# Performance work log

Hardware: AMD Instinct MI355X
Metric: run time of the kernel (lower is better)

The kernel has to match this reference:

```python
import jax, jax.numpy as jnp
import numpy as np

N, E, F_IN, H, C, G, NCLS, L = 50000, 600000, 128, 4, 64, 64, 3, 3
HC = H * C  # 256


def gatv2_layer(x, src, dst, Wl, bl, Wr, br, att, bias):
    # PyG GATv2Conv (concat=True, negative_slope=0.2, share_weights=False),
    # eval mode so attention dropout is identity.
    n = x.shape[0]
    xl = (x @ Wl + bl).reshape(n, H, C)  # source transform
    xr = (x @ Wr + br).reshape(n, H, C)  # target transform
    e = jax.nn.leaky_relu(xl[src] + xr[dst], negative_slope=0.2)  # [E',H,C]
    score = jnp.einsum('ehc,hc->eh', e, att)                      # [E',H]
    # softmax over incoming edges of each destination node
    mx = jax.ops.segment_max(score, dst, num_segments=n)
    ex = jnp.exp(score - mx[dst])
    denom = jax.ops.segment_sum(ex, dst, num_segments=n)
    alpha = ex / denom[dst]                                       # [E',H]
    out = jax.ops.segment_sum(alpha[..., None] * xl[src], dst, num_segments=n)
    return out.reshape(n, HC) + bias


def setup_inputs() -> dict:
    key = jax.random.key(0)
    ks = jax.random.split(key, 32)
    d = {}
    d['x'] = jax.random.normal(ks[0], (N, F_IN), dtype=jnp.float32)
    d['edge_index'] = jax.random.randint(ks[1], (2, E), 0, N, dtype=jnp.int64)
    d['batch'] = jnp.sort(jax.random.randint(ks[2], (N,), 0, G, dtype=jnp.int64))
    k = 3
    for li in range(L):
        fin = F_IN if li == 0 else HC
        s = 1.0 / np.sqrt(fin)
        d[f'Wl{li}'] = jax.random.normal(ks[k], (fin, HC), dtype=jnp.float32) * s; k += 1
        d[f'bl{li}'] = jnp.zeros((HC,), dtype=jnp.float32)
        d[f'Wr{li}'] = jax.random.normal(ks[k], (fin, HC), dtype=jnp.float32) * s; k += 1
        d[f'br{li}'] = jnp.zeros((HC,), dtype=jnp.float32)
        d[f'att{li}'] = jax.random.normal(ks[k], (H, C), dtype=jnp.float32) * (1.0 / np.sqrt(C)); k += 1
        d[f'bias{li}'] = jnp.zeros((HC,), dtype=jnp.float32)
    d['Wout'] = jax.random.normal(ks[k], (HC, NCLS), dtype=jnp.float32) * (1.0 / np.sqrt(HC))
    d['bout'] = jnp.zeros((NCLS,), dtype=jnp.float32)
    return d


def reference(x, edge_index, batch,
              Wl0, bl0, Wr0, br0, att0, bias0,
              Wl1, bl1, Wr1, br1, att1, bias1,
              Wl2, bl2, Wr2, br2, att2, bias2,
              Wout, bout):
    # add self loops (add_self_loops=True)
    loops = jnp.arange(N, dtype=edge_index.dtype)
    src = jnp.concatenate([edge_index[0], loops])
    dst = jnp.concatenate([edge_index[1], loops])

    h = gatv2_layer(x, src, dst, Wl0, bl0, Wr0, br0, att0, bias0)
    for (Wl, bl, Wr, br, att, bias) in [(Wl1, bl1, Wr1, br1, att1, bias1),
                                        (Wl2, bl2, Wr2, br2, att2, bias2)]:
        h = jax.nn.relu(h)
        h = gatv2_layer(h, src, dst, Wl, bl, Wr, br, att, bias)

    # pooling=0: mean + max over graphs
    counts = jax.ops.segment_sum(jnp.ones((N,), dtype=h.dtype), batch, num_segments=G)
    mean_p = jax.ops.segment_sum(h, batch, num_segments=G) / jnp.maximum(counts, 1.0)[:, None]
    max_p = jax.ops.segment_max(h, batch, num_segments=G)
    p = mean_p + max_p
    # dropout is identity in eval mode
    logits = p @ Wout + bout
    return jax.nn.softmax(logits, axis=1)
```

## Files before the change

### kernel.cpp

```cpp
#include <hip/hip_runtime.h>
#include <math.h>

#define N_NODES 50000
#define N_EDGES 600000
#define F_INPUT 128
#define HCDIM 256
#define NGRAPH 64
#define NCLS 3
#define MPAD 50048
#define SCAN_NB ((N_NODES + 255) / 256)
#define LOG2E 1.4426950408889634f
#define NPART 32

#define SPLITX_NB (MPAD * F_INPUT / 4 / 256)
#define ZERO_NB   (((MPAD - N_NODES) * HCDIM / 4 + 255) / 256)
#define WPREP_NB  (512 * (F_INPUT + HCDIM + HCDIM) / 256)
#define PREP_NB   (SPLITX_NB + ZERO_NB + WPREP_NB)
#define HIST_NB   ((N_EDGES + N_NODES + 255) / 256)
#define BND_NB    ((N_NODES + 255) / 256)

typedef float f32x4 __attribute__((ext_vector_type(4)));
typedef float f32x2 __attribute__((ext_vector_type(2)));
typedef _Float16 f16x8 __attribute__((ext_vector_type(8)));
typedef _Float16 f16x4 __attribute__((ext_vector_type(4)));
typedef _Float16 h2 __attribute__((ext_vector_type(2)));

__device__ __forceinline__ void gl_lds16(const void* g, void* l) {
    __builtin_amdgcn_global_load_lds(
        (const __attribute__((address_space(1))) unsigned int*)g,
        (__attribute__((address_space(3))) unsigned int*)l, 16, 0, 0);
}

__device__ __forceinline__ h2 bch2(unsigned int u) { return __builtin_bit_cast(h2, u); }
__device__ __forceinline__ h2 pk16(float a, float b) {
    return __builtin_bit_cast(h2, __builtin_amdgcn_cvt_pkrtz(a, b));
}

__device__ __forceinline__ h2 lrelu2(h2 v) {
    const h2 z = {(_Float16)0.f, (_Float16)0.f};
    const h2 c = {(_Float16)0.2f, (_Float16)0.2f};
    h2 mx = __builtin_elementwise_max(v, z);
    h2 mn = __builtin_elementwise_min(v, z);
    return mx + mn * c;
}

__global__ void hist_boundary_kernel(const int* __restrict__ ei, int* __restrict__ deg,
                                     const int* __restrict__ batch,
                                     int* __restrict__ startg, int* __restrict__ endg) {
    int b = blockIdx.x;
    if (b < HIST_NB) {
        int i = b * 256 + threadIdx.x;
        int total = N_EDGES + N_NODES;
        if (i >= total) return;
        int d = (i < N_EDGES) ? ei[N_EDGES + i] : (i - N_EDGES);
        atomicAdd(&deg[d], 1);
    } else {
        int i = (b - HIST_NB) * 256 + threadIdx.x;
        if (i >= N_NODES) return;
        int g = batch[i];
        if (i == 0 || batch[i - 1] != g) startg[g] = i;
        if (i == N_NODES - 1 || batch[i + 1] != g) endg[g] = i + 1;
    }
}

__global__ void block_scan_kernel(const int* __restrict__ deg, int* __restrict__ rowptr,
                                  int* __restrict__ bsums) {
    __shared__ int wt[4];
    int b = blockIdx.x, t = threadIdx.x, lane = t & 63, wid = t >> 6;
    int i = b * 256 + t;
    int v = (i < N_NODES) ? deg[i] : 0;
    int x = v;
    #pragma unroll
    for (int off = 1; off < 64; off <<= 1) {
        int y = __shfl_up(x, off, 64);
        if (lane >= off) x += y;
    }
    if (lane == 63) wt[wid] = x;
    __syncthreads();
    if (t == 0) {
        int s = 0;
        #pragma unroll
        for (int j = 0; j < 4; ++j) { int tv = wt[j]; wt[j] = s; s += tv; }
        bsums[b] = s;
    }
    __syncthreads();
    if (i < N_NODES) rowptr[i] = wt[wid] + x - v;
}

__global__ void add_off_kernel(int* __restrict__ rowptr, int* __restrict__ cursor,
                               const int* __restrict__ bsums) {
    __shared__ int red[256];
    int b = blockIdx.x, t = threadIdx.x;
    red[t] = (t < b) ? bsums[t] : 0;
    __syncthreads();
    for (int off = 128; off > 0; off >>= 1) {
        if (t < off) red[t] += red[t + off];
        __syncthreads();
    }
    int offv = red[0];
    int i = b * 256 + t;
    if (i < N_NODES) {
        int r = rowptr[i] + offv;
        rowptr[i] = r;
        cursor[i] = r;
    }
    if (i == 0) rowptr[N_NODES] = N_EDGES + N_NODES;
}

__global__ void fill_kernel(const int* __restrict__ ei, int* __restrict__ cursor,
                            int* __restrict__ colx) {
    int i = blockIdx.x * 256 + threadIdx.x;
    int total = N_EDGES + N_NODES;
    if (i >= total + 8) return;
    if (i >= total) { colx[i] = 0; return; }
    int s, d;
    if (i < N_EDGES) { s = ei[i]; d = ei[N_EDGES + i]; }
    else             { s = i - N_EDGES; d = s; }
    int pos = atomicAdd(&cursor[d], 1);
    colx[pos] = s * HCDIM;
}

__global__ void prep_kernel(const float* __restrict__ x, _Float16* __restrict__ A,
                            _Float16* __restrict__ Bt0, _Float16* __restrict__ Bt1,
                            _Float16* __restrict__ Bt2,
                            const float* __restrict__ Wl0, const float* __restrict__ Wr0,
                            const float* __restrict__ Wl1, const float* __restrict__ Wr1,
                            const float* __restrict__ Wl2, const float* __restrict__ Wr2) {
    int b = blockIdx.x;
    if (b < SPLITX_NB) {
        int base = (b * 256 + threadIdx.x) * 4;
        int row = base >> 7;
        float4 v = make_float4(0.f, 0.f, 0.f, 0.f);
        if (row < N_NODES) v = *(const float4*)&x[base];
        f16x4 o;
        o.x = (_Float16)v.x; o.y = (_Float16)v.y; o.z = (_Float16)v.z; o.w = (_Float16)v.w;
        *(f16x4*)&A[base] = o;
    } else if (b < SPLITX_NB + ZERO_NB) {
        int i = ((b - SPLITX_NB) * 256 + threadIdx.x) * 4;
        if (i < (MPAD - N_NODES) * HCDIM) {
            f16x4 z = {(_Float16)0.f, (_Float16)0.f, (_Float16)0.f, (_Float16)0.f};
            *(f16x4*)&A[(size_t)N_NODES * HCDIM + i] = z;
        }
    } else {
        int t = (b - SPLITX_NB - ZERO_NB) * 256 + threadIdx.x;
        const float* Wl; const float* Wr; _Float16* Bt; int K;
        if (t < 512 * F_INPUT)            { Wl = Wl0; Wr = Wr0; Bt = Bt0; K = F_INPUT; }
        else if (t < 512 * (F_INPUT + HCDIM)) { t -= 512 * F_INPUT; Wl = Wl1; Wr = Wr1; Bt = Bt1; K = HCDIM; }
        else                              { t -= 512 * (F_INPUT + HCDIM); Wl = Wl2; Wr = Wr2; Bt = Bt2; K = HCDIM; }
        int n = t & 511, k = t >> 9;
        float w = (n < 256) ? Wl[k * 256 + n] : Wr[k * 256 + (n - 256)];
        Bt[n * K + k] = (_Float16)w;
    }
}

__global__ __launch_bounds__(256) void gemm_mfma(
    const _Float16* __restrict__ A, const _Float16* __restrict__ B,
    int K,
    const float* __restrict__ bl, const float* __restrict__ br,
    unsigned char* __restrict__ xl8, _Float16* __restrict__ xrh)
{
    __shared__ _Float16 sA[64 * 64], sB[128 * 64];
    int tid = threadIdx.x;
    int lane = tid & 63, wave = tid >> 6;
    int wm = wave >> 1, wn = wave & 1;
    int bx = blockIdx.x >> 2, by = blockIdx.x & 3;
    int row0 = bx * 64;
    int n0 = by * 128;
    int quad = lane >> 4, l16 = lane & 15;

    f32x4 acc[2][4];
    #pragma unroll
    for (int i = 0; i < 2; ++i)
        #pragma unroll
        for (int j = 0; j < 4; ++j)
            acc[i][j] = (f32x4){0.f, 0.f, 0.f, 0.f};

    for (int k0 = 0; k0 < K; k0 += 64) {
        __syncthreads();
        #pragma unroll
        for (int pass = 0; pass < 2; ++pass) {
            int c = tid + pass * 256;
            int r = c >> 3;
            int pl = c & 7;
            int pg = pl ^ (r & 7);
            size_t ga = (size_t)(row0 + r) * K + k0 + pg * 8;
            gl_lds16(A + ga, sA + c * 8);
        }
        #pragma unroll
        for (int pass = 0; pass < 4; ++pass) {
            int c = tid + pass * 256;
            int r = c >> 3;
            int pl = c & 7;
            int pg = pl ^ (r & 7);
            size_t gb = (size_t)(n0 + r) * K + k0 + pg * 8;
            gl_lds16(B + gb, sB + c * 8);
        }
        __syncthreads();

        #pragma unroll
        for (int kk = 0; kk < 2; ++kk) {
            f16x8 fa[2], fb[4];
            #pragma unroll
            for (int i = 0; i < 2; ++i) {
                int rr = wm * 32 + i * 16 + l16;
                int ca = (kk * 4 + quad) ^ (rr & 7);
                fa[i] = *(const f16x8*)&sA[rr * 64 + ca * 8];
            }
            #pragma unroll
            for (int j = 0; j < 4; ++j) {
                int nn = wn * 64 + j * 16 + l16;
                int cb = (kk * 4 + quad) ^ (nn & 7);
                fb[j] = *(const f16x8*)&sB[nn * 64 + cb * 8];
            }
            #pragma unroll
            for (int i = 0; i < 2; ++i)
                #pragma unroll
                for (int j = 0; j < 4; ++j)
                    acc[i][j] = __builtin_amdgcn_mfma_f32_16x16x32_f16(fa[i], fb[j], acc[i][j], 0, 0, 0);
        }
    }

    if (by < 2) {
        int cb0 = by * 128;
        #pragma unroll
        for (int j = 0; j < 4; ++j) {
            int col = cb0 + wn * 64 + j * 16 + l16;
            float bj = bl[col];
            #pragma unroll
            for (int i = 0; i < 2; ++i) {
                int rbase = row0 + wm * 32 + i * 16 + quad * 4;
                #pragma unroll
                for (int r = 0; r < 4; ++r) {
                    int row = rbase + r;
                    if (row < N_NODES) {
                        float v = acc[i][j][r] + bj;
                        int pk = __builtin_amdgcn_cvt_pk_fp8_f32(v, v, 0, false);
                        xl8[(size_t)row * HCDIM + col] = (unsigned char)pk;
                    }
                }
            }
        }
    } else {
        int cb0 = (by - 2) * 128;
        #pragma unroll
        for (int j = 0; j < 4; ++j) {
            int col = cb0 + wn * 64 + j * 16 + l16;
            float bj = br[col];
            #pragma unroll
            for (int i = 0; i < 2; ++i) {
                int rbase = row0 + wm * 32 + i * 16 + quad * 4;
                #pragma unroll
                for (int r = 0; r < 4; ++r) {
                    int row = rbase + r;
                    if (row < N_NODES)
                        xrh[(size_t)row * HCDIM + col] = (_Float16)(acc[i][j][r] + bj);
                }
            }
        }
    }
}

__global__ __launch_bounds__(256) void gat_edge(
    const unsigned char* __restrict__ xl8, const _Float16* __restrict__ xrh,
    const float* __restrict__ att, const float* __restrict__ bias,
    const int* __restrict__ rowptr, const int* __restrict__ colx,
    _Float16* __restrict__ outh, _Float16* __restrict__ onext, int mode)
{
    int wave = threadIdx.x >> 6;
    int lane = threadIdx.x & 63;
    int q  = lane >> 4;
    int ql = lane & 15;
    int node = blockIdx.x * 4 + wave;
    if (node >= N_NODES) return;
    int cb = ql * 16;

    const char* xrrow = (const char*)xrh + (size_t)node * (HCDIM * 2) + cb * 2;
    uint4 xu0 = *(const uint4*)xrrow;
    uint4 xu1 = *(const uint4*)(xrrow + 16);
    h2 xr[8] = { bch2(xu0.x), bch2(xu0.y), bch2(xu0.z), bch2(xu0.w),
                 bch2(xu1.x), bch2(xu1.y), bch2(xu1.z), bch2(xu1.w) };
    h2 at[8];
    #pragma unroll
    for (int i = 0; i < 8; ++i) {
        float2 av = *(const float2*)&att[cb + i * 2];
        at[i] = (h2){(_Float16)(av.x * LOG2E), (_Float16)(av.y * LOG2E)};
    }

    int e0 = rowptr[node], e1 = rowptr[node + 1];
    float denom = 0.f;
    float acc[16];
    #pragma unroll
    for (int i = 0; i < 16; ++i) acc[i] = 0.f;

    uint4 d = *(const uint4*)(xl8 + (unsigned)(colx[e0 + q] + cb));

    for (int e = e0; e < e1; e += 4) {
        uint4 nd = *(const uint4*)(xl8 + (unsigned)(colx[e + 4 + q] + cb));

        unsigned int dw[4] = {d.x, d.y, d.z, d.w};
        f32x2 flo[4], fhi[4];
        h2 hx[8];
        #pragma unroll
        for (int j = 0; j < 4; ++j) {
            flo[j] = __builtin_amdgcn_cvt_pk_f32_fp8(dw[j], false);
            fhi[j] = __builtin_amdgcn_cvt_pk_f32_fp8(dw[j], true);
            hx[2 * j]     = pk16(flo[j].x, flo[j].y);
            hx[2 * j + 1] = pk16(fhi[j].x, fhi[j].y);
        }
        float pa = 0.f, pb = 0.f;
        #pragma unroll
        for (int i = 0; i < 4; ++i) {
            pa = __builtin_amdgcn_fdot2(lrelu2(hx[i] + xr[i]), at[i], pa, false);
            pb = __builtin_amdgcn_fdot2(lrelu2(hx[i + 4] + xr[i + 4]), at[i + 4], pb, false);
        }
        float p = pa + pb;
        p += __builtin_bit_cast(float, __builtin_amdgcn_ds_swizzle(__builtin_bit_cast(int, p), 0x041F));
        p += __builtin_bit_cast(float, __builtin_amdgcn_ds_swizzle(__builtin_bit_cast(int, p), 0x081F));

        float w;
        if (e + 4 <= e1) {
            w = exp2f(p);
        } else {
            w = (e + q < e1) ? exp2f(p) : 0.f;
        }
        denom += w;
        #pragma unroll
        for (int j = 0; j < 4; ++j) {
            acc[4 * j]     += w * flo[j].x;
            acc[4 * j + 1] += w * flo[j].y;
            acc[4 * j + 2] += w * fhi[j].x;
            acc[4 * j + 3] += w * fhi[j].y;
        }
        d = nd;
    }

    denom += __shfl_xor(denom, 16, 64);
    denom += __shfl_xor(denom, 32, 64);
    #pragma unroll
    for (int i = 0; i < 16; ++i) {
        acc[i] += __shfl_xor(acc[i], 16, 64);
        acc[i] += __shfl_xor(acc[i], 32, 64);
    }

    if (q == 0) {
        float inv = 1.f / denom;
        char* orow = (char*)(mode == 0 ? outh : onext) + (size_t)node * (HCDIM * 2) + cb * 2;
        h2 o[8];
        #pragma unroll
        for (int i = 0; i < 8; ++i) {
            float2 bv = *(const float2*)&bias[cb + i * 2];
            float v0 = acc[2 * i] * inv + bv.x;
            float v1 = acc[2 * i + 1] * inv + bv.y;
            if (mode != 0) { v0 = fmaxf(v0, 0.f); v1 = fmaxf(v1, 0.f); }
            o[i] = pk16(v0, v1);
        }
        uint4 s0 = { __builtin_bit_cast(unsigned int, o[0]), __builtin_bit_cast(unsigned int, o[1]),
                     __builtin_bit_cast(unsigned int, o[2]), __builtin_bit_cast(unsigned int, o[3]) };
        uint4 s1 = { __builtin_bit_cast(unsigned int, o[4]), __builtin_bit_cast(unsigned int, o[5]),
                     __builtin_bit_cast(unsigned int, o[6]), __builtin_bit_cast(unsigned int, o[7]) };
        *(uint4*)orow = s0;
        *(uint4*)(orow + 16) = s1;
    }
}

__global__ __launch_bounds__(256) void pool_partial(
    const _Float16* __restrict__ h, const int* __restrict__ startg,
    const int* __restrict__ endg, float* __restrict__ sumP, float* __restrict__ maxP)
{
    __shared__ float4 sS[4][64];
    __shared__ float4 sM[4][64];
    int g = blockIdx.x >> 5, part = blockIdx.x & (NPART - 1);
    int lane = threadIdx.x & 63;
    int sub = threadIdx.x >> 6;
    int c0 = lane * 4;
    int s = startg[g], e = endg[g];
    float4 sum = make_float4(0.f, 0.f, 0.f, 0.f);
    float4 mx = make_float4(-INFINITY, -INFINITY, -INFINITY, -INFINITY);
    for (int i = s + part * 4 + sub; i < e; i += NPART * 4) {
        uint2 u = *(const uint2*)&h[(size_t)i * HCDIM + c0];
        h2 a = bch2(u.x), b = bch2(u.y);
        float4 v = make_float4((float)a.x, (float)a.y, (float)b.x, (float)b.y);
        sum.x += v.x; sum.y += v.y; sum.z += v.z; sum.w += v.w;
        mx.x = fmaxf(mx.x, v.x); mx.y = fmaxf(mx.y, v.y);
        mx.z = fmaxf(mx.z, v.z); mx.w = fmaxf(mx.w, v.w);
    }
    sS[sub][lane] = sum; sM[sub][lane] = mx;
    __syncthreads();
    if (sub == 0) {
        #pragma unroll
        for (int j = 1; j < 4; ++j) {
            float4 a = sS[j][lane], b = sM[j][lane];
            sum.x += a.x; sum.y += a.y; sum.z += a.z; sum.w += a.w;
            mx.x = fmaxf(mx.x, b.x); mx.y = fmaxf(mx.y, b.y);
            mx.z = fmaxf(mx.z, b.z); mx.w = fmaxf(mx.w, b.w);
        }
        size_t o = (size_t)blockIdx.x * HCDIM + c0;
        *(float4*)&sumP[o] = sum;
        *(float4*)&maxP[o] = mx;
    }
}

__global__ __launch_bounds__(256) void pool_final_logits(
    const float* __restrict__ sumP, const float* __restrict__ maxP,
    const int* __restrict__ startg, const int* __restrict__ endg,
    const float* __restrict__ Wout, const float* __restrict__ bout,
    float* __restrict__ out)
{
    __shared__ float red[256];
    __shared__ float lg[NCLS];
    int g = blockIdx.x, c = threadIdx.x;
    float s = 0.f, m = -INFINITY;
    #pragma unroll 8
    for (int part = 0; part < NPART; ++part) {
        size_t o = (size_t)(g * NPART + part) * HCDIM + c;
        s += sumP[o];
        m = fmaxf(m, maxP[o]);
    }
    int cnt = endg[g] - startg[g];
    float inv = 1.f / fmaxf((float)cnt, 1.f);
    float pv = s * inv + m;

    for (int j = 0; j < NCLS; ++j) {
        red[c] = pv * Wout[c * NCLS + j];
        __syncthreads();
        for (int off = 128; off > 0; off >>= 1) {
            if (c < off) red[c] += red[c + off];
            __syncthreads();
        }
        if (c == 0) lg[j] = red[0] + bout[j];
        __syncthreads();
    }
    if (c == 0) {
        float mx = fmaxf(lg[0], fmaxf(lg[1], lg[2]));
        float e0 = __expf(lg[0] - mx), e1 = __expf(lg[1] - mx), e2 = __expf(lg[2] - mx);
        float invs = 1.f / (e0 + e1 + e2);
        out[g * NCLS + 0] = e0 * invs;
        out[g * NCLS + 1] = e1 * invs;
        out[g * NCLS + 2] = e2 * invs;
    }
}

extern "C" void kernel_launch(void* const* d_in, const int* in_sizes, int n_in,
                              void* d_out, int out_size, void* d_ws, size_t ws_size,
                              hipStream_t stream) {
    const float* x     = (const float*)d_in[0];
    const int*   ei    = (const int*)d_in[1];
    const int*   batch = (const int*)d_in[2];
    const float *Wl[3], *bl[3], *Wr[3], *br[3], *att[3], *bias[3];
    for (int li = 0; li < 3; ++li) {
        int b = 3 + li * 6;
        Wl[li]   = (const float*)d_in[b + 0];
        bl[li]   = (const float*)d_in[b + 1];
        Wr[li]   = (const float*)d_in[b + 2];
        br[li]   = (const float*)d_in[b + 3];
        att[li]  = (const float*)d_in[b + 4];
        bias[li] = (const float*)d_in[b + 5];
    }
    const float* Wout = (const float*)d_in[21];
    const float* bout = (const float*)d_in[22];
    float* out = (float*)d_out;

    size_t off = 0;
    char* wsb = (char*)d_ws;
    auto alloc = [&](size_t bytes) -> char* {
        char* ptr = wsb + off;
        off += (bytes + 255) & ~(size_t)255;
        return ptr;
    };
    int* zblk    = (int*)alloc((N_NODES + 2 * NGRAPH) * sizeof(int));
    int* deg     = zblk;
    int* startg  = zblk + N_NODES;
    int* endg    = zblk + N_NODES + NGRAPH;
    int* rowptr  = (int*)alloc((N_NODES + 1) * sizeof(int));
    int* cursor  = (int*)alloc(N_NODES * sizeof(int));
    int* bsums   = (int*)alloc(256 * sizeof(int));
    int* colx    = (int*)alloc((size_t)(N_EDGES + N_NODES + 8) * sizeof(int));
    _Float16* Abuf = (_Float16*)alloc((size_t)MPAD * HCDIM * sizeof(_Float16));
    _Float16* Bt[3];
    for (int li = 0; li < 3; ++li) {
        int K = (li == 0) ? F_INPUT : HCDIM;
        Bt[li] = (_Float16*)alloc((size_t)512 * K * sizeof(_Float16));
    }
    unsigned char* xl8 = (unsigned char*)alloc((size_t)N_NODES * HCDIM);
    _Float16* xrh  = (_Float16*)alloc((size_t)N_NODES * HCDIM * sizeof(_Float16));
    _Float16* hbuf = (_Float16*)alloc((size_t)N_NODES * HCDIM * sizeof(_Float16));
    float* sumP    = (float*)alloc((size_t)NGRAPH * NPART * HCDIM * sizeof(float));
    float* maxP    = (float*)alloc((size_t)NGRAPH * NPART * HCDIM * sizeof(float));

    hipMemsetAsync(zblk, 0, (N_NODES + 2 * NGRAPH) * sizeof(int), stream);

    hist_boundary_kernel<<<HIST_NB + BND_NB, 256, 0, stream>>>(ei, deg, batch, startg, endg);
    block_scan_kernel<<<SCAN_NB, 256, 0, stream>>>(deg, rowptr, bsums);
    add_off_kernel<<<SCAN_NB, 256, 0, stream>>>(rowptr, cursor, bsums);
    fill_kernel<<<(N_EDGES + N_NODES + 8 + 255) / 256, 256, 0, stream>>>(ei, cursor, colx);

    prep_kernel<<<PREP_NB, 256, 0, stream>>>(x, Abuf, Bt[0], Bt[1], Bt[2],
                                             Wl[0], Wr[0], Wl[1], Wr[1], Wl[2], Wr[2]);

    for (int li = 0; li < 3; ++li) {
        int K = (li == 0) ? F_INPUT : HCDIM;
        gemm_mfma<<<(MPAD / 64) * 4, 256, 0, stream>>>(
            Abuf, Bt[li], K, bl[li], br[li], xl8, xrh);
        if (li < 2) {
            gat_edge<<<N_NODES / 4, 256, 0, stream>>>(
                xl8, xrh, att[li], bias[li], rowptr, colx, nullptr, Abuf, 1);
        } else {
            gat_edge<<<N_NODES / 4, 256, 0, stream>>>(
                xl8, xrh, att[li], bias[li], rowptr, colx, hbuf, nullptr, 0);
        }
    }

    pool_partial<<<NGRAPH * NPART, 256, 0, stream>>>(hbuf, startg, endg, sumP, maxP);
    pool_final_logits<<<NGRAPH, 256, 0, stream>>>(sumP, maxP, startg, endg, Wout, bout, out);
}
```

Baseline: 451.1 us.

## Load GEMM fragments directly from global and stage epilogue through LDS

The MFMA GEMM no longer stages A and B tiles in LDS with global_load_lds and barriers. Each lane now loads its f16x8 fragments straight from global memory, which drops the per-K-step syncs but gives up LDS reuse and leans on L1/L2 for the repeated reads. The epilogue now writes results into a shared buffer and then does coalesced 16-byte row stores for both the fp8 xl output and the fp16 xr output. This replaces the scattered per-element byte and half stores.

```diff
diff --git a/kernel.cpp b/kernel.cpp
--- a/kernel.cpp
+++ b/kernel.cpp
@@ -24,12 +24,6 @@
 typedef _Float16 f16x8 __attribute__((ext_vector_type(8)));
 typedef _Float16 f16x4 __attribute__((ext_vector_type(4)));
 typedef _Float16 h2 __attribute__((ext_vector_type(2)));
-
-__device__ __forceinline__ void gl_lds16(const void* g, void* l) {
-    __builtin_amdgcn_global_load_lds(
-        (const __attribute__((address_space(1))) unsigned int*)g,
-        (__attribute__((address_space(3))) unsigned int*)l, 16, 0, 0);
-}
 
 __device__ __forceinline__ h2 bch2(unsigned int u) { return __builtin_bit_cast(h2, u); }
 __device__ __forceinline__ h2 pk16(float a, float b) {
@@ -159,14 +153,20 @@
     const float* __restrict__ bl, const float* __restrict__ br,
     unsigned char* __restrict__ xl8, _Float16* __restrict__ xrh)
 {
-    __shared__ _Float16 sA[64 * 64], sB[128 * 64];
+    __shared__ char sC[16384];
     int tid = threadIdx.x;
     int lane = tid & 63, wave = tid >> 6;
     int wm = wave >> 1, wn = wave & 1;
     int bx = blockIdx.x >> 2, by = blockIdx.x & 3;
-    int row0 = bx * 64;
-    int n0 = by * 128;
+    int row0 = bx * 64, n0 = by * 128;
     int quad = lane >> 4, l16 = lane & 15;
+
+    const _Float16* Ar0 = A + (size_t)(row0 + wm * 32 + l16) * K + quad * 8;
+    const _Float16* Ar1 = Ar0 + (size_t)16 * K;
+    const _Float16* Br[4];
+    #pragma unroll
+    for (int j = 0; j < 4; ++j)
+        Br[j] = B + (size_t)(n0 + wn * 64 + j * 16 + l16) * K + quad * 8;
 
     f32x4 acc[2][4];
     #pragma unroll
@@ -175,87 +175,70 @@
         for (int j = 0; j < 4; ++j)
             acc[i][j] = (f32x4){0.f, 0.f, 0.f, 0.f};
 
-    for (int k0 = 0; k0 < K; k0 += 64) {
-        __syncthreads();
-        #pragma unroll
-        for (int pass = 0; pass < 2; ++pass) {
-            int c = tid + pass * 256;
-            int r = c >> 3;
-            int pl = c & 7;
-            int pg = pl ^ (r & 7);
-            size_t ga = (size_t)(row0 + r) * K + k0 + pg * 8;
-            gl_lds16(A + ga, sA + c * 8);
-        }
-        #pragma unroll
-        for (int pass = 0; pass < 4; ++pass) {
-            int c = tid + pass * 256;
-            int r = c >> 3;
-            int pl = c & 7;
-            int pg = pl ^ (r & 7);
-            size_t gb = (size_t)(n0 + r) * K + k0 + pg * 8;
-            gl_lds16(B + gb, sB + c * 8);
-        }
-        __syncthreads();
-
-        #pragma unroll
-        for (int kk = 0; kk < 2; ++kk) {
-            f16x8 fa[2], fb[4];
+    for (int k0 = 0; k0 < K; k0 += 32) {
+        f16x8 fa0 = *(const f16x8*)(Ar0 + k0);
+        f16x8 fa1 = *(const f16x8*)(Ar1 + k0);
+        f16x8 fb[4];
+        #pragma unroll
+        for (int j = 0; j < 4; ++j)
+            fb[j] = *(const f16x8*)(Br[j] + k0);
+        #pragma unroll
+        for (int j = 0; j < 4; ++j) {
+            acc[0][j] = __builtin_amdgcn_mfma_f32_16x16x32_f16(fa0, fb[j], acc[0][j], 0, 0, 0);
+            acc[1][j] = __builtin_amdgcn_mfma_f32_16x16x32_f16(fa1, fb[j], acc[1][j], 0, 0, 0);
+        }
+    }
+
+    if (by < 2) {
+        unsigned char* s8 = (unsigned char*)sC;
+        int cb0 = by * 128;
+        #pragma unroll
+        for (int j = 0; j < 4; ++j) {
+            int coll = wn * 64 + j * 16 + l16;
+            float bj = bl[cb0 + coll];
             #pragma unroll
             for (int i = 0; i < 2; ++i) {
-                int rr = wm * 32 + i * 16 + l16;
-                int ca = (kk * 4 + quad) ^ (rr & 7);
-                fa[i] = *(const f16x8*)&sA[rr * 64 + ca * 8];
+                int rl = wm * 32 + i * 16 + quad * 4;
+                #pragma unroll
+                for (int r = 0; r < 4; ++r) {
+                    float v = acc[i][j][r] + bj;
+                    s8[(rl + r) * 128 + coll] =
+                        (unsigned char)__builtin_amdgcn_cvt_pk_fp8_f32(v, v, 0, false);
+                }
             }
-            #pragma unroll
-            for (int j = 0; j < 4; ++j) {
-                int nn = wn * 64 + j * 16 + l16;
-                int cb = (kk * 4 + quad) ^ (nn & 7);
-                fb[j] = *(const f16x8*)&sB[nn * 64 + cb * 8];
-            }
-            #pragma unroll
-            for (int i = 0; i < 2; ++i)
-                #pragma unroll
-                for (int j = 0; j < 4; ++j)
-                    acc[i][j] = __builtin_amdgcn_mfma_f32_16x16x32_f16(fa[i], fb[j], acc[i][j], 0, 0, 0);
-        }
-    }
-
-    if (by < 2) {
-        int cb0 = by * 128;
+        }
+        __syncthreads();
+        int rl = tid >> 2, seg = (tid & 3) * 32;
+        int grow = row0 + rl;
+        if (grow < N_NODES) {
+            uint4 v0 = *(const uint4*)&s8[rl * 128 + seg];
+            uint4 v1 = *(const uint4*)&s8[rl * 128 + seg + 16];
+            *(uint4*)&xl8[(size_t)grow * HCDIM + cb0 + seg] = v0;
+            *(uint4*)&xl8[(size_t)grow * HCDIM + cb0 + seg + 16] = v1;
+        }
+    } else {
+        _Float16* s16 = (_Float16*)sC;
+        int cb0 = (by - 2) * 128;
         #pragma unroll
         for (int j = 0; j < 4; ++j) {
-            int col = cb0 + wn * 64 + j * 16 + l16;
-            float bj = bl[col];
+            int coll = wn * 64 + j * 16 + l16;
+            float bj = br[cb0 + coll];
             #pragma unroll
             for (int i = 0; i < 2; ++i) {
-                int rbase = row0 + wm * 32 + i * 16 + quad * 4;
+                int rl = wm * 32 + i * 16 + quad * 4;
                 #pragma unroll
-                for (int r = 0; r < 4; ++r) {
-                    int row = rbase + r;
-                    if (row < N_NODES) {
-                        float v = acc[i][j][r] + bj;
-                        int pk = __builtin_amdgcn_cvt_pk_fp8_f32(v, v, 0, false);
-                        xl8[(size_t)row * HCDIM + col] = (unsigned char)pk;
-                    }
-                }
+                for (int r = 0; r < 4; ++r)
+                    s16[(rl + r) * 128 + coll] = (_Float16)(acc[i][j][r] + bj);
             }
         }
-    } else {
-        int cb0 = (by - 2) * 128;
-        #pragma unroll
-        for (int j = 0; j < 4; ++j) {
-            int col = cb0 + wn * 64 + j * 16 + l16;
-            float bj = br[col];
-            #pragma unroll
-            for (int i = 0; i < 2; ++i) {
-                int rbase = row0 + wm * 32 + i * 16 + quad * 4;
-                #pragma unroll
-                for (int r = 0; r < 4; ++r) {
-                    int row = rbase + r;
-                    if (row < N_NODES)
-                        xrh[(size_t)row * HCDIM + col] = (_Float16)(acc[i][j][r] + bj);
-                }
-            }
+        __syncthreads();
+        int rl = tid >> 2, segE = (tid & 3) * 32;
+        int grow = row0 + rl;
+        if (grow < N_NODES) {
+            const uint4* src = (const uint4*)&s16[rl * 128 + segE];
+            uint4 a0 = src[0], a1 = src[1], a2 = src[2], a3 = src[3];
+            uint4* dst = (uint4*)&xrh[(size_t)grow * HCDIM + cb0 + segE];
+            dst[0] = a0; dst[1] = a1; dst[2] = a2; dst[3] = a3;
         }
     }
 }
```

After: 548.9 us. 21.7% more time.
